# Kernel tuning notes

Hardware: AMD Instinct MI355X
Metric: run time of the kernel (lower is better)

The kernel has to match this reference:

```python
import jax, jax.numpy as jnp
import numpy as np

N_NODES = 50000
N_EDGES = 800000
N_GRAPHS = 128
IN, HID, OUT, CLS = 128, 128, 128, 10


def setup_inputs() -> dict:
    key = jax.random.key(0)
    ks = jax.random.split(key, 16)
    d = {}
    d["features"] = jax.random.normal(ks[0], (N_NODES, IN), jnp.float32)
    d["edge_src"] = jax.random.randint(ks[1], (N_EDGES,), 0, N_NODES)
    d["edge_dst"] = jax.random.randint(ks[2], (N_EDGES,), 0, N_NODES)
    d["graph_ids"] = jnp.sort(jax.random.randint(ks[3], (N_NODES,), 0, N_GRAPHS))

    def lin(k, i, o):
        return (jax.random.normal(k, (i, o), jnp.float32) / np.float32(np.sqrt(i)))

    dims = [(IN, HID), (HID, HID), (HID, OUT)]
    for l, (i, o) in enumerate(dims):
        d[f"Ws{l}"] = lin(ks[4 + 3 * l], i, o)
        d[f"Wn{l}"] = lin(ks[5 + 3 * l], i, o)
        d[f"b{l}"] = jnp.zeros((o,), jnp.float32)
    d["Wf"] = lin(ks[13], OUT, CLS)
    d["bf"] = jnp.zeros((CLS,), jnp.float32)
    return d


def _sage_mean_layer(h, edge_src, edge_dst, Ws, Wn, b, in_deg):
    # mean-aggregate in-neighbor features: gather at src, segment-sum at dst
    msg_sum = jax.ops.segment_sum(h[edge_src], edge_dst, num_segments=N_NODES)
    h_neigh = msg_sum / in_deg  # [N, d], zero-degree nodes divide by 1 -> 0
    return jax.nn.relu(h @ Ws + h_neigh @ Wn + b)


def reference(features, edge_src, edge_dst, graph_ids,
              Ws0, Wn0, b0, Ws1, Wn1, b1, Ws2, Wn2, b2, Wf, bf):
    ones = jnp.ones((N_EDGES,), jnp.float32)
    in_deg = jax.ops.segment_sum(ones, edge_dst, num_segments=N_NODES)
    in_deg = jnp.maximum(in_deg, 1.0)[:, None]  # [N, 1]

    h = features
    h = _sage_mean_layer(h, edge_src, edge_dst, Ws0, Wn0, b0, in_deg)
    h = _sage_mean_layer(h, edge_src, edge_dst, Ws1, Wn1, b1, in_deg)
    h = _sage_mean_layer(h, edge_src, edge_dst, Ws2, Wn2, b2, in_deg)

    # mean graph pooling over node segments
    node_ones = jnp.ones((N_NODES,), jnp.float32)
    counts = jax.ops.segment_sum(node_ones, graph_ids, num_segments=N_GRAPHS)
    counts = jnp.maximum(counts, 1.0)[:, None]
    pooled = jax.ops.segment_sum(h, graph_ids, num_segments=N_GRAPHS) / counts

    return pooled @ Wf + bf  # [N_GRAPHS, CLS]
```

## Files before the change

### kernel.cpp

```cpp
#include <hip/hip_runtime.h>

#define N_NODES  50000
#define N_EDGES  800000
#define N_GRAPHS 128
#define HD       128
#define K2       256
#define CLS      10
#define NB_SCAN  ((N_NODES + 255) / 256)
#define NPART    8
#define PSIZE    (N_NODES / NPART)
#define NBIN     1600
#define CHUNK    (N_EDGES / NBIN)
#define PCAP     131072

typedef __attribute__((ext_vector_type(8))) _Float16 f16x8;
typedef __attribute__((ext_vector_type(4))) float f32x4;
typedef __attribute__((ext_vector_type(2))) float f32x2;

union U4H8 { uint4 u; _Float16 h[8]; };
union U2H4 { uint2 u; _Float16 h[4]; };

typedef const __attribute__((address_space(1))) void* gptr_t;
typedef __attribute__((address_space(3))) void* lptr_t;
#define GLOAD_LDS16(g, l) \
    __builtin_amdgcn_global_load_lds((gptr_t)(g), (lptr_t)(l), 16, 0, 0)

__global__ __launch_bounds__(256) void k_zero(int* __restrict__ z) {
    int i = blockIdx.x * 256 + threadIdx.x;
    if (i < 50008) z[i] = 0;
}

__global__ __launch_bounds__(256) void k_initbin(
    const float* __restrict__ f, unsigned short* __restrict__ c0, unsigned char* __restrict__ f8,
    const float* __restrict__ Ws0, const float* __restrict__ Wn0,
    const float* __restrict__ Ws1, const float* __restrict__ Wn1,
    const float* __restrict__ Ws2, const float* __restrict__ Wn2,
    unsigned short* __restrict__ wt, float* __restrict__ pooled,
    const int* __restrict__ gid, float* __restrict__ counts, int* __restrict__ bflag,
    const int* __restrict__ src, const int* __restrict__ dst,
    unsigned* __restrict__ stag, int* __restrict__ gcount, int* __restrict__ deg) {
    if (blockIdx.x < NBIN) {
        __shared__ int lcount[NPART];
        __shared__ int lbase[NPART];
        const int tid = threadIdx.x;
        const int lo = blockIdx.x * CHUNK;
        if (tid < NPART) lcount[tid] = 0;
        __syncthreads();
        int dc[2], sc[2];
#pragma unroll
        for (int it = 0; it < 2; ++it) {
            int i = lo + tid + it * 256;
            dc[it] = -1;
            if (i < lo + CHUNK) {
                int d = dst[i];
                dc[it] = d; sc[it] = src[i];
                atomicAdd(&deg[d], 1);
                atomicAdd(&lcount[d / PSIZE], 1);
            }
        }
        __syncthreads();
        if (tid < NPART) {
            lbase[tid] = atomicAdd(&gcount[tid], lcount[tid]);
            lcount[tid] = 0;
        }
        __syncthreads();
#pragma unroll
        for (int it = 0; it < 2; ++it) {
            if (dc[it] >= 0) {
                int p = dc[it] / PSIZE;
                int slot = atomicAdd(&lcount[p], 1);
                stag[(size_t)p * PCAP + lbase[p] + slot] =
                    (unsigned)sc[it] | ((unsigned)(dc[it] - p * PSIZE) << 16);
            }
        }
        return;
    }
    long long gi = (long long)(blockIdx.x - NBIN) * 256 + threadIdx.x;
    if (gi < 800000) {
        int t = (int)gi;
        int row = t >> 4, c8 = (t & 15) * 8;
        const float* p = f + (size_t)row * HD + c8;
        float4 a = *(const float4*)p;
        float4 b = *(const float4*)(p + 4);
        U4H8 v;
        v.h[0] = (_Float16)a.x; v.h[1] = (_Float16)a.y;
        v.h[2] = (_Float16)a.z; v.h[3] = (_Float16)a.w;
        v.h[4] = (_Float16)b.x; v.h[5] = (_Float16)b.y;
        v.h[6] = (_Float16)b.z; v.h[7] = (_Float16)b.w;
        *(uint4*)(c0 + (size_t)row * K2 + c8) = v.u;
        int p0 = __builtin_amdgcn_cvt_pk_fp8_f32(a.x, a.y, 0, false);
        p0 = __builtin_amdgcn_cvt_pk_fp8_f32(a.z, a.w, p0, true);
        int p1 = __builtin_amdgcn_cvt_pk_fp8_f32(b.x, b.y, 0, false);
        p1 = __builtin_amdgcn_cvt_pk_fp8_f32(b.z, b.w, p1, true);
        *(uint2*)(f8 + (size_t)row * HD + c8) = make_uint2((unsigned)p0, (unsigned)p1);
        return;
    }
    gi -= 800000;
    if (gi < 3 * HD * K2) {
        int t = (int)gi;
        int l = t / (HD * K2), r = t % (HD * K2);
        int n = r / K2, k = r % K2;
        const float* Ws = (l == 0) ? Ws0 : (l == 1) ? Ws1 : Ws2;
        const float* Wn = (l == 0) ? Wn0 : (l == 1) ? Wn1 : Wn2;
        float w = (k < HD) ? Ws[k * HD + n] : Wn[(k - HD) * HD + n];
        union { unsigned short u; _Float16 h; } c;
        c.h = (_Float16)w;
        wt[t] = c.u;
        return;
    }
    gi -= 3 * HD * K2;
    if (gi < N_GRAPHS * HD) { pooled[gi] = 0.f; return; }
    gi -= (long long)N_GRAPHS * HD;
    if (gi < N_GRAPHS) {
        int g = (int)gi;
        int lo = 0, hi = N_NODES;
        while (lo < hi) { int mid = (lo + hi) >> 1; if (gid[mid] < g) lo = mid + 1; else hi = mid; }
        int start = lo;
        lo = 0; hi = N_NODES;
        while (lo < hi) { int mid = (lo + hi) >> 1; if (gid[mid] <= g) lo = mid + 1; else hi = mid; }
        counts[g] = (float)(lo - start);
        return;
    }
    gi -= N_GRAPHS;
    if (gi < 256) bflag[gi] = 0;
}
#define INIT_ITEMS (800000 + 3 * HD * K2 + N_GRAPHS * HD + N_GRAPHS + 256)
#define INIT_BLOCKS ((INIT_ITEMS + 255) / 256)

__global__ __launch_bounds__(256) void k_scan(const int* __restrict__ deg,
                                              int* __restrict__ rowptr, int* __restrict__ cursor,
                                              int* __restrict__ bsum, int* __restrict__ bflag) {
    __shared__ int s[256];
    __shared__ int r[256];
    const int tid = threadIdx.x;
    const int b = blockIdx.x;
    const int i = b * 256 + tid;
    int v = (i < N_NODES) ? deg[i] : 0;
    s[tid] = v;
    __syncthreads();
    for (int off = 1; off < 256; off <<= 1) {
        int add = (tid >= off) ? s[tid - off] : 0;
        __syncthreads();
        s[tid] += add;
        __syncthreads();
    }
    if (tid == 255) {
        __hip_atomic_store(&bsum[b], s[255], __ATOMIC_RELAXED, __HIP_MEMORY_SCOPE_AGENT);
        __hip_atomic_store(&bflag[b], 1, __ATOMIC_RELEASE, __HIP_MEMORY_SCOPE_AGENT);
    }
    int agg = 0;
    if (tid < b) {
        while (__hip_atomic_load(&bflag[tid], __ATOMIC_ACQUIRE, __HIP_MEMORY_SCOPE_AGENT) == 0) {}
        agg = __hip_atomic_load(&bsum[tid], __ATOMIC_RELAXED, __HIP_MEMORY_SCOPE_AGENT);
    }
    r[tid] = agg;
    __syncthreads();
    for (int off = 128; off > 0; off >>= 1) {
        if (tid < off) r[tid] += r[tid + off];
        __syncthreads();
    }
    if (i < N_NODES) {
        int val = r[0] + s[tid] - v;
        rowptr[i] = val;
        cursor[i] = val;
    }
    if (b == NB_SCAN - 1 && tid == 0) rowptr[N_NODES] = N_EDGES;
}

__global__ __launch_bounds__(256) void k_fill2(const unsigned* __restrict__ stag, const int* __restrict__ gcount,
                                               int* __restrict__ cursor, int* __restrict__ eidx) {
    const int part = blockIdx.x & (NPART - 1);
    const int blk = blockIdx.x >> 3;
    const int n = gcount[part];
    const unsigned* s = stag + (size_t)part * PCAP;
    for (int i = blk * 256 + threadIdx.x; i < n; i += 64 * 256) {
        unsigned v = s[i];
        int srcv = (int)(v & 0xFFFFu);
        int dstv = part * PSIZE + (int)(v >> 16);
        int pos = atomicAdd(&cursor[dstv], 1);
        eidx[pos] = srcv;
    }
}

__global__ __launch_bounds__(256) void k_gather(const unsigned char* __restrict__ h8,
                                                const int* __restrict__ rowptr,
                                                const int* __restrict__ eidx,
                                                unsigned short* __restrict__ msg) {
    const int node = (blockIdx.x * 256 + threadIdx.x) >> 6;
    const int lane = threadIdx.x & 63;
    if (node >= N_NODES) return;
    const int epar = lane >> 4;
    const int d0 = (lane & 15) * 8;
    const int beg = rowptr[node], end = rowptr[node + 1];
    float acc[8] = {0.f, 0.f, 0.f, 0.f, 0.f, 0.f, 0.f, 0.f};
    int j = beg + epar;
    for (; j + 12 < end; j += 16) {
        int s0 = eidx[j], s1 = eidx[j + 4], s2 = eidx[j + 8], s3 = eidx[j + 12];
        uint2 v0 = *(const uint2*)(h8 + (size_t)s0 * HD + d0);
        uint2 v1 = *(const uint2*)(h8 + (size_t)s1 * HD + d0);
        uint2 v2 = *(const uint2*)(h8 + (size_t)s2 * HD + d0);
        uint2 v3 = *(const uint2*)(h8 + (size_t)s3 * HD + d0);
        f32x2 e;
        e = __builtin_amdgcn_cvt_pk_f32_fp8(v0.x, false); acc[0] += e[0]; acc[1] += e[1];
        e = __builtin_amdgcn_cvt_pk_f32_fp8(v0.x, true);  acc[2] += e[0]; acc[3] += e[1];
        e = __builtin_amdgcn_cvt_pk_f32_fp8(v0.y, false); acc[4] += e[0]; acc[5] += e[1];
        e = __builtin_amdgcn_cvt_pk_f32_fp8(v0.y, true);  acc[6] += e[0]; acc[7] += e[1];
        e = __builtin_amdgcn_cvt_pk_f32_fp8(v1.x, false); acc[0] += e[0]; acc[1] += e[1];
        e = __builtin_amdgcn_cvt_pk_f32_fp8(v1.x, true);  acc[2] += e[0]; acc[3] += e[1];
        e = __builtin_amdgcn_cvt_pk_f32_fp8(v1.y, false); acc[4] += e[0]; acc[5] += e[1];
        e = __builtin_amdgcn_cvt_pk_f32_fp8(v1.y, true);  acc[6] += e[0]; acc[7] += e[1];
        e = __builtin_amdgcn_cvt_pk_f32_fp8(v2.x, false); acc[0] += e[0]; acc[1] += e[1];
        e = __builtin_amdgcn_cvt_pk_f32_fp8(v2.x, true);  acc[2] += e[0]; acc[3] += e[1];
        e = __builtin_amdgcn_cvt_pk_f32_fp8(v2.y, false); acc[4] += e[0]; acc[5] += e[1];
        e = __builtin_amdgcn_cvt_pk_f32_fp8(v2.y, true);  acc[6] += e[0]; acc[7] += e[1];
        e = __builtin_amdgcn_cvt_pk_f32_fp8(v3.x, false); acc[0] += e[0]; acc[1] += e[1];
        e = __builtin_amdgcn_cvt_pk_f32_fp8(v3.x, true);  acc[2] += e[0]; acc[3] += e[1];
        e = __builtin_amdgcn_cvt_pk_f32_fp8(v3.y, false); acc[4] += e[0]; acc[5] += e[1];
        e = __builtin_amdgcn_cvt_pk_f32_fp8(v3.y, true);  acc[6] += e[0]; acc[7] += e[1];
    }
    for (; j < end; j += 4) {
        uint2 v0 = *(const uint2*)(h8 + (size_t)eidx[j] * HD + d0);
        f32x2 e;
        e = __builtin_amdgcn_cvt_pk_f32_fp8(v0.x, false); acc[0] += e[0]; acc[1] += e[1];
        e = __builtin_amdgcn_cvt_pk_f32_fp8(v0.x, true);  acc[2] += e[0]; acc[3] += e[1];
        e = __builtin_amdgcn_cvt_pk_f32_fp8(v0.y, false); acc[4] += e[0]; acc[5] += e[1];
        e = __builtin_amdgcn_cvt_pk_f32_fp8(v0.y, true);  acc[6] += e[0]; acc[7] += e[1];
    }
#pragma unroll
    for (int i = 0; i < 8; ++i) {
        acc[i] += __shfl_xor(acc[i], 16);
        acc[i] += __shfl_xor(acc[i], 32);
    }
    if (epar == 0) {
        float inv = (end > beg) ? 1.0f / (float)(end - beg) : 0.f;
        U4H8 o;
#pragma unroll
        for (int i = 0; i < 8; ++i) o.h[i] = (_Float16)(acc[i] * inv);
        *(uint4*)(msg + (size_t)node * K2 + HD + d0) = o.u;
    }
}

__global__ __launch_bounds__(256) void k_sage(const unsigned short* __restrict__ hin,
                                              const unsigned short* __restrict__ wt,
                                              const float* __restrict__ bias,
                                              unsigned short* __restrict__ hout,
                                              unsigned char* __restrict__ hout8,
                                              int write16) {
    __shared__ __align__(16) _Float16 Ah[2][128 * 64];
    __shared__ __align__(16) _Float16 Bw[2][128 * 64];
    const int tid = threadIdx.x;
    const int wv = tid >> 6, lane = tid & 63;
    const int m0 = blockIdx.x * 128;
    const int m_off = (wv >> 1) * 64, n_off = (wv & 1) * 64;
    const int l15 = lane & 15, q = lane >> 4;

    f32x4 acc[4][4];
#pragma unroll
    for (int a = 0; a < 4; ++a)
#pragma unroll
        for (int b = 0; b < 4; ++b) acc[a][b] = (f32x4){0.f, 0.f, 0.f, 0.f};

    auto stage = [&](int bsel, int kt) {
        const int k0 = kt * 64;
#pragma unroll
        for (int i = 0; i < 4; ++i) {
            int idx = tid + i * 256;
            int row = idx >> 3, c = idx & 7;
            int qs = (c ^ (row & 7)) * 8;
            int gm = m0 + row;
            if (gm < N_NODES)
                GLOAD_LDS16(hin + (size_t)gm * K2 + k0 + qs, &Ah[bsel][idx * 8]);
            GLOAD_LDS16(wt + (size_t)row * K2 + k0 + qs, &Bw[bsel][idx * 8]);
        }
    };

    stage(0, 0);
    __syncthreads();
#pragma unroll
    for (int kt = 0; kt < 4; ++kt) {
        const int b = kt & 1;
        if (kt < 3) stage(b ^ 1, kt + 1);
        f16x8 hf[4][2], wf[4][2];
#pragma unroll
        for (int mt = 0; mt < 4; ++mt) {
            const int row = m_off + mt * 16 + l15;
            const int sw = row & 7;
#pragma unroll
            for (int ks = 0; ks < 2; ++ks)
                hf[mt][ks] = *(const f16x8*)&Ah[b][row * 64 + (((ks * 4 + q) ^ sw) * 8)];
        }
#pragma unroll
        for (int nt = 0; nt < 4; ++nt) {
            const int row = n_off + nt * 16 + l15;
            const int sw = row & 7;
#pragma unroll
            for (int ks = 0; ks < 2; ++ks)
                wf[nt][ks] = *(const f16x8*)&Bw[b][row * 64 + (((ks * 4 + q) ^ sw) * 8)];
        }
#pragma unroll
        for (int mt = 0; mt < 4; ++mt)
#pragma unroll
            for (int nt = 0; nt < 4; ++nt) {
                acc[mt][nt] = __builtin_amdgcn_mfma_f32_16x16x32_f16(wf[nt][0], hf[mt][0], acc[mt][nt], 0, 0, 0);
                acc[mt][nt] = __builtin_amdgcn_mfma_f32_16x16x32_f16(wf[nt][1], hf[mt][1], acc[mt][nt], 0, 0, 0);
            }
        __syncthreads();
    }
#pragma unroll
    for (int nt = 0; nt < 4; ++nt) {
        int n = n_off + nt * 16 + q * 4;
        float4 bv = *(const float4*)(bias + n);
#pragma unroll
        for (int mt = 0; mt < 4; ++mt) {
            int m = m0 + m_off + mt * 16 + l15;
            if (m < N_NODES) {
                f32x4 a = acc[mt][nt];
                float r0 = fmaxf(a[0] + bv.x, 0.f);
                float r1 = fmaxf(a[1] + bv.y, 0.f);
                float r2 = fmaxf(a[2] + bv.z, 0.f);
                float r3 = fmaxf(a[3] + bv.w, 0.f);
                if (write16) {
                    U2H4 v;
                    v.h[0] = (_Float16)r0; v.h[1] = (_Float16)r1;
                    v.h[2] = (_Float16)r2; v.h[3] = (_Float16)r3;
                    *(uint2*)(hout + (size_t)m * K2 + n) = v.u;
                }
                int p = __builtin_amdgcn_cvt_pk_fp8_f32(r0, r1, 0, false);
                p = __builtin_amdgcn_cvt_pk_fp8_f32(r2, r3, p, true);
                *(unsigned int*)(hout8 + (size_t)m * HD + n) = (unsigned)p;
            }
        }
    }
}

__global__ __launch_bounds__(256) void k_pool(const unsigned char* __restrict__ h8,
                                              const int* __restrict__ gid,
                                              float* __restrict__ pooled) {
    const int p2 = (threadIdx.x & 63) * 2;
    const int sl = threadIdx.x >> 6;
    const int n0 = blockIdx.x * 128;
    float a0 = 0.f, a1 = 0.f;
    int cur = -1;
    for (int i = sl; i < 128; i += 4) {
        int n = n0 + i;
        if (n >= N_NODES) break;
        int g = gid[n];
        if (g != cur) {
            if (cur >= 0) {
                atomicAdd(&pooled[(size_t)cur * HD + p2], a0);
                atomicAdd(&pooled[(size_t)cur * HD + p2 + 1], a1);
            }
            a0 = 0.f; a1 = 0.f;
            cur = g;
        }
        unsigned short v = *(const unsigned short*)(h8 + (size_t)n * HD + p2);
        f32x2 e = __builtin_amdgcn_cvt_pk_f32_fp8((unsigned)v, false);
        a0 += e[0]; a1 += e[1];
    }
    if (cur >= 0) {
        atomicAdd(&pooled[(size_t)cur * HD + p2], a0);
        atomicAdd(&pooled[(size_t)cur * HD + p2 + 1], a1);
    }
}

__global__ __launch_bounds__(256) void k_final(const float* __restrict__ pooled,
                                               const float* __restrict__ counts,
                                               const float* __restrict__ Wf,
                                               const float* __restrict__ bf,
                                               float* __restrict__ out) {
    int t = blockIdx.x * 256 + threadIdx.x;
    if (t >= N_GRAPHS * CLS) return;
    int g = t / CLS, c = t % CLS;
    float inv = 1.0f / fmaxf(counts[g], 1.0f);
    float s = 0.f;
    for (int k = 0; k < HD; ++k) s += pooled[(size_t)g * HD + k] * Wf[k * CLS + c];
    out[t] = s * inv + bf[c];
}

extern "C" void kernel_launch(void* const* d_in, const int* in_sizes, int n_in,
                              void* d_out, int out_size, void* d_ws, size_t ws_size,
                              hipStream_t stream) {
    const float* features = (const float*)d_in[0];
    const int*   esrc     = (const int*)d_in[1];
    const int*   edst     = (const int*)d_in[2];
    const int*   gids     = (const int*)d_in[3];
    const float* bs[3]  = {(const float*)d_in[6], (const float*)d_in[9], (const float*)d_in[12]};
    const float* Wf = (const float*)d_in[13];
    const float* bfv = (const float*)d_in[14];
    float* out = (float*)d_out;

    int* deg_i  = (int*)d_ws;
    int* gcount = deg_i + 50000;
    int* rowptr = deg_i + 50064;
    int* cursor = rowptr + 50064;
    int* bsum   = cursor + 50048;
    int* bflag  = bsum + 256;
    int* eidx   = bflag + 256;
    unsigned* stag = (unsigned*)(eidx + 800000);
    float* pooled = (float*)(stag + (size_t)NPART * PCAP);
    float* counts = pooled + N_GRAPHS * HD;
    unsigned short* C0 = (unsigned short*)(counts + 128);
    unsigned short* C1 = C0 + (size_t)N_NODES * K2;
    unsigned short* C2 = C1 + (size_t)N_NODES * K2;
    unsigned short* Wt = C2 + (size_t)N_NODES * K2;
    unsigned char* F0 = (unsigned char*)(Wt + 3 * HD * K2);
    unsigned char* F1 = F0 + (size_t)N_NODES * HD;
    unsigned char* F2 = F1 + (size_t)N_NODES * HD;

    k_zero<<<196, 256, 0, stream>>>(deg_i);

    k_initbin<<<NBIN + INIT_BLOCKS, 256, 0, stream>>>(
        features, C0, F0,
        (const float*)d_in[4], (const float*)d_in[5],
        (const float*)d_in[7], (const float*)d_in[8],
        (const float*)d_in[10], (const float*)d_in[11],
        Wt, pooled, gids, counts, bflag,
        esrc, edst, stag, gcount, deg_i);

    k_scan<<<NB_SCAN, 256, 0, stream>>>(deg_i, rowptr, cursor, bsum, bflag);
    k_fill2<<<NPART * 64, 256, 0, stream>>>(stag, gcount, cursor, eidx);

    unsigned short* C[4] = {C0, C1, C2, C0};
    unsigned char* F[4] = {F0, F1, F2, F0};
    for (int l = 0; l < 3; ++l) {
        k_gather<<<(N_NODES * 64 + 255) / 256, 256, 0, stream>>>(F[l], rowptr, eidx, C[l]);
        k_sage<<<(N_NODES + 127) / 128, 256, 0, stream>>>(
            C[l], Wt + (size_t)l * HD * K2, bs[l], C[l + 1], F[l + 1], (l < 2) ? 1 : 0);
    }

    k_pool<<<(N_NODES + 127) / 128, 256, 0, stream>>>(F0, gids, pooled);
    k_final<<<(N_GRAPHS * CLS + 255) / 256, 256, 0, stream>>>(pooled, counts, Wf, bfv, out);
}
```

Measured before the change: 339.4 us.

## Build CSR per partition sub-range with LDS histograms instead of global degree atomics

Removes the global degree atomics, the decoupled-lookback scan kernel and the global-cursor fill kernel. In their place, one k_build kernel runs 64 blocks, one per (partition, sub-range) pair. Each block scans its whole partition's staged edges twice: once to build an LDS histogram and count the edges that fall before its range, then to scatter source indices using LDS atomics. This cuts launches and global atomic traffic, but each block rereads its partition's edge list (about 100k entries) twice, and only 64 blocks are active.

```diff
diff --git a/kernel.cpp b/kernel.cpp
--- a/kernel.cpp
+++ b/kernel.cpp
@@ -6,9 +6,10 @@
 #define HD       128
 #define K2       256
 #define CLS      10
-#define NB_SCAN  ((N_NODES + 255) / 256)
 #define NPART    8
 #define PSIZE    (N_NODES / NPART)
+#define SUB      8
+#define SUBSZ    784
 #define NBIN     1600
 #define CHUNK    (N_EDGES / NBIN)
 #define PCAP     131072
@@ -25,9 +26,8 @@
 #define GLOAD_LDS16(g, l) \
     __builtin_amdgcn_global_load_lds((gptr_t)(g), (lptr_t)(l), 16, 0, 0)
 
-__global__ __launch_bounds__(256) void k_zero(int* __restrict__ z) {
-    int i = blockIdx.x * 256 + threadIdx.x;
-    if (i < 50008) z[i] = 0;
+__global__ __launch_bounds__(64) void k_zero(int* __restrict__ z) {
+    if (threadIdx.x < 8) z[threadIdx.x] = 0;
 }
 
 __global__ __launch_bounds__(256) void k_initbin(
@@ -36,9 +36,9 @@
     const float* __restrict__ Ws1, const float* __restrict__ Wn1,
     const float* __restrict__ Ws2, const float* __restrict__ Wn2,
     unsigned short* __restrict__ wt, float* __restrict__ pooled,
-    const int* __restrict__ gid, float* __restrict__ counts, int* __restrict__ bflag,
+    const int* __restrict__ gid, float* __restrict__ counts,
     const int* __restrict__ src, const int* __restrict__ dst,
-    unsigned* __restrict__ stag, int* __restrict__ gcount, int* __restrict__ deg) {
+    unsigned* __restrict__ stag, int* __restrict__ gcount) {
     if (blockIdx.x < NBIN) {
         __shared__ int lcount[NPART];
         __shared__ int lbase[NPART];
@@ -54,7 +54,6 @@
             if (i < lo + CHUNK) {
                 int d = dst[i];
                 dc[it] = d; sc[it] = src[i];
-                atomicAdd(&deg[d], 1);
                 atomicAdd(&lcount[d / PSIZE], 1);
             }
         }
@@ -119,67 +118,98 @@
         lo = 0; hi = N_NODES;
         while (lo < hi) { int mid = (lo + hi) >> 1; if (gid[mid] <= g) lo = mid + 1; else hi = mid; }
         counts[g] = (float)(lo - start);
-        return;
-    }
-    gi -= N_GRAPHS;
-    if (gi < 256) bflag[gi] = 0;
-}
-#define INIT_ITEMS (800000 + 3 * HD * K2 + N_GRAPHS * HD + N_GRAPHS + 256)
+    }
+}
+#define INIT_ITEMS (800000 + 3 * HD * K2 + N_GRAPHS * HD + N_GRAPHS)
 #define INIT_BLOCKS ((INIT_ITEMS + 255) / 256)
 
-__global__ __launch_bounds__(256) void k_scan(const int* __restrict__ deg,
-                                              int* __restrict__ rowptr, int* __restrict__ cursor,
-                                              int* __restrict__ bsum, int* __restrict__ bflag) {
-    __shared__ int s[256];
-    __shared__ int r[256];
+__global__ __launch_bounds__(512) void k_build(const unsigned* __restrict__ stag,
+                                               const int* __restrict__ gcount,
+                                               int* __restrict__ rowptr, int* __restrict__ eidx) {
+    __shared__ int hist[SUBSZ];
+    __shared__ int sc[512];
+    __shared__ int before_sh;
+    __shared__ int base_sh;
     const int tid = threadIdx.x;
-    const int b = blockIdx.x;
-    const int i = b * 256 + tid;
-    int v = (i < N_NODES) ? deg[i] : 0;
-    s[tid] = v;
+    const int p = blockIdx.x & (NPART - 1);
+    const int s = blockIdx.x >> 3;
+    const int lo = s * SUBSZ;
+    const int hi = min(lo + SUBSZ, PSIZE);
+    for (int j = tid; j < SUBSZ; j += 512) hist[j] = 0;
+    if (tid == 0) {
+        int b = 0;
+        for (int q = 0; q < p; ++q) b += gcount[q];
+        base_sh = b;
+        before_sh = 0;
+    }
     __syncthreads();
-    for (int off = 1; off < 256; off <<= 1) {
-        int add = (tid >= off) ? s[tid - off] : 0;
-        __syncthreads();
-        s[tid] += add;
-        __syncthreads();
-    }
-    if (tid == 255) {
-        __hip_atomic_store(&bsum[b], s[255], __ATOMIC_RELAXED, __HIP_MEMORY_SCOPE_AGENT);
-        __hip_atomic_store(&bflag[b], 1, __ATOMIC_RELEASE, __HIP_MEMORY_SCOPE_AGENT);
-    }
-    int agg = 0;
-    if (tid < b) {
-        while (__hip_atomic_load(&bflag[tid], __ATOMIC_ACQUIRE, __HIP_MEMORY_SCOPE_AGENT) == 0) {}
-        agg = __hip_atomic_load(&bsum[tid], __ATOMIC_RELAXED, __HIP_MEMORY_SCOPE_AGENT);
-    }
-    r[tid] = agg;
+    const int n = gcount[p];
+    const unsigned* sp = stag + (size_t)p * PCAP;
+    int bef = 0;
+    const int nmain = (n / 2048) * 2048;
+    for (int i = tid; i < nmain; i += 2048) {
+        unsigned v0 = sp[i], v1 = sp[i + 512], v2 = sp[i + 1024], v3 = sp[i + 1536];
+#pragma unroll
+        for (int u = 0; u < 4; ++u) {
+            int off = (int)((u == 0 ? v0 : u == 1 ? v1 : u == 2 ? v2 : v3) >> 16);
+            if (off >= lo && off < hi) atomicAdd(&hist[off - lo], 1);
+            bef += (off < lo) ? 1 : 0;
+        }
+    }
+    for (int i = nmain + tid; i < n; i += 512) {
+        int off = (int)(sp[i] >> 16);
+        if (off >= lo && off < hi) atomicAdd(&hist[off - lo], 1);
+        bef += (off < lo) ? 1 : 0;
+    }
+#pragma unroll
+    for (int d = 1; d < 64; d <<= 1) bef += __shfl_xor(bef, d);
+    if ((tid & 63) == 0 && bef) atomicAdd(&before_sh, bef);
     __syncthreads();
-    for (int off = 128; off > 0; off >>= 1) {
-        if (tid < off) r[tid] += r[tid + off];
-        __syncthreads();
-    }
-    if (i < N_NODES) {
-        int val = r[0] + s[tid] - v;
-        rowptr[i] = val;
-        cursor[i] = val;
-    }
-    if (b == NB_SCAN - 1 && tid == 0) rowptr[N_NODES] = N_EDGES;
-}
-
-__global__ __launch_bounds__(256) void k_fill2(const unsigned* __restrict__ stag, const int* __restrict__ gcount,
-                                               int* __restrict__ cursor, int* __restrict__ eidx) {
-    const int part = blockIdx.x & (NPART - 1);
-    const int blk = blockIdx.x >> 3;
-    const int n = gcount[part];
-    const unsigned* s = stag + (size_t)part * PCAP;
-    for (int i = blk * 256 + threadIdx.x; i < n; i += 64 * 256) {
-        unsigned v = s[i];
-        int srcv = (int)(v & 0xFFFFu);
-        int dstv = part * PSIZE + (int)(v >> 16);
-        int pos = atomicAdd(&cursor[dstv], 1);
-        eidx[pos] = srcv;
-    }
+    const int T2 = tid * 2;
+    int lsum = 0;
+    if (T2 < SUBSZ) lsum = hist[T2] + hist[T2 + 1];
+    sc[tid] = lsum;
+    __syncthreads();
+    for (int off = 1; off < 512; off <<= 1) {
+        int add = (tid >= off) ? sc[tid - off] : 0;
+        __syncthreads();
+        sc[tid] += add;
+        __syncthreads();
+    }
+    const int run0 = sc[tid] - lsum;
+    const int B = base_sh + before_sh;
+    if (T2 < SUBSZ) {
+        int h0 = hist[T2];
+        int h1 = hist[T2 + 1];
+        hist[T2] = run0;
+        hist[T2 + 1] = run0 + h0;
+        int n0 = lo + T2, n1 = lo + T2 + 1;
+        if (n0 < PSIZE) rowptr[p * PSIZE + n0] = B + run0;
+        if (n1 < PSIZE) rowptr[p * PSIZE + n1] = B + run0 + h0;
+        (void)h1;
+    }
+    __syncthreads();
+    for (int i = tid; i < nmain; i += 2048) {
+        unsigned v0 = sp[i], v1 = sp[i + 512], v2 = sp[i + 1024], v3 = sp[i + 1536];
+#pragma unroll
+        for (int u = 0; u < 4; ++u) {
+            unsigned v = (u == 0 ? v0 : u == 1 ? v1 : u == 2 ? v2 : v3);
+            int off = (int)(v >> 16);
+            if (off >= lo && off < hi) {
+                int slot = atomicAdd(&hist[off - lo], 1);
+                eidx[B + slot] = (int)(v & 0xFFFFu);
+            }
+        }
+    }
+    for (int i = nmain + tid; i < n; i += 512) {
+        unsigned v = sp[i];
+        int off = (int)(v >> 16);
+        if (off >= lo && off < hi) {
+            int slot = atomicAdd(&hist[off - lo], 1);
+            eidx[B + slot] = (int)(v & 0xFFFFu);
+        }
+    }
+    if (blockIdx.x == 8 * SUB - 1 && tid == 0) rowptr[N_NODES] = N_EDGES;
 }
 
 __global__ __launch_bounds__(256) void k_gather(const unsigned char* __restrict__ h8,
@@ -389,13 +419,9 @@
     const float* bfv = (const float*)d_in[14];
     float* out = (float*)d_out;
 
-    int* deg_i  = (int*)d_ws;
-    int* gcount = deg_i + 50000;
-    int* rowptr = deg_i + 50064;
-    int* cursor = rowptr + 50064;
-    int* bsum   = cursor + 50048;
-    int* bflag  = bsum + 256;
-    int* eidx   = bflag + 256;
+    int* gcount = (int*)d_ws;
+    int* rowptr = gcount + 8;
+    int* eidx   = rowptr + 50008;
     unsigned* stag = (unsigned*)(eidx + 800000);
     float* pooled = (float*)(stag + (size_t)NPART * PCAP);
     float* counts = pooled + N_GRAPHS * HD;
@@ -407,18 +433,17 @@
     unsigned char* F1 = F0 + (size_t)N_NODES * HD;
     unsigned char* F2 = F1 + (size_t)N_NODES * HD;
 
-    k_zero<<<196, 256, 0, stream>>>(deg_i);
+    k_zero<<<1, 64, 0, stream>>>(gcount);
 
     k_initbin<<<NBIN + INIT_BLOCKS, 256, 0, stream>>>(
         features, C0, F0,
         (const float*)d_in[4], (const float*)d_in[5],
         (const float*)d_in[7], (const float*)d_in[8],
         (const float*)d_in[10], (const float*)d_in[11],
-        Wt, pooled, gids, counts, bflag,
-        esrc, edst, stag, gcount, deg_i);
-
-    k_scan<<<NB_SCAN, 256, 0, stream>>>(deg_i, rowptr, cursor, bsum, bflag);
-    k_fill2<<<NPART * 64, 256, 0, stream>>>(stag, gcount, cursor, eidx);
+        Wt, pooled, gids, counts,
+        esrc, edst, stag, gcount);
+
+    k_build<<<NPART * SUB, 512, 0, stream>>>(stag, gcount, rowptr, eidx);
 
     unsigned short* C[4] = {C0, C1, C2, C0};
     unsigned char* F[4] = {F0, F1, F2, F0};
```

Measured after the change: 319.5 us. -5.9%, faster.

## Build CSR via per-partition LDS histograms and LDS-cursor scatter

Applied to the files above, without the earlier changes.

Replaces the global degree atomics and global-cursor atomic fill with a two-pass counting sort. Each of 128 blocks (8 partitions × 16 sub-chunks) first builds a shared-memory histogram of destination offsets. The scan then sums those histograms and writes per-block starting cursors. The scatter pass uses shared-memory atomics for slot assignment, removing contended global atomics. In exchange it adds a kernel, a large ghist buffer, and extra reads of the staged edges, with only 128 blocks doing the work.

```diff
diff --git a/kernel.cpp b/kernel.cpp
--- a/kernel.cpp
+++ b/kernel.cpp
@@ -6,9 +6,10 @@
 #define HD       128
 #define K2       256
 #define CLS      10
-#define NB_SCAN  ((N_NODES + 255) / 256)
 #define NPART    8
 #define PSIZE    (N_NODES / NPART)
+#define NSUB     16
+#define NB_SCAN  ((N_NODES + 255) / 256)
 #define NBIN     1600
 #define CHUNK    (N_EDGES / NBIN)
 #define PCAP     131072
@@ -25,9 +26,8 @@
 #define GLOAD_LDS16(g, l) \
     __builtin_amdgcn_global_load_lds((gptr_t)(g), (lptr_t)(l), 16, 0, 0)
 
-__global__ __launch_bounds__(256) void k_zero(int* __restrict__ z) {
-    int i = blockIdx.x * 256 + threadIdx.x;
-    if (i < 50008) z[i] = 0;
+__global__ __launch_bounds__(64) void k_zero(int* __restrict__ z) {
+    if (threadIdx.x < 8) z[threadIdx.x] = 0;
 }
 
 __global__ __launch_bounds__(256) void k_initbin(
@@ -38,7 +38,7 @@
     unsigned short* __restrict__ wt, float* __restrict__ pooled,
     const int* __restrict__ gid, float* __restrict__ counts, int* __restrict__ bflag,
     const int* __restrict__ src, const int* __restrict__ dst,
-    unsigned* __restrict__ stag, int* __restrict__ gcount, int* __restrict__ deg) {
+    unsigned* __restrict__ stag, int* __restrict__ gcount) {
     if (blockIdx.x < NBIN) {
         __shared__ int lcount[NPART];
         __shared__ int lbase[NPART];
@@ -54,7 +54,6 @@
             if (i < lo + CHUNK) {
                 int d = dst[i];
                 dc[it] = d; sc[it] = src[i];
-                atomicAdd(&deg[d], 1);
                 atomicAdd(&lcount[d / PSIZE], 1);
             }
         }
@@ -127,25 +126,54 @@
 #define INIT_ITEMS (800000 + 3 * HD * K2 + N_GRAPHS * HD + N_GRAPHS + 256)
 #define INIT_BLOCKS ((INIT_ITEMS + 255) / 256)
 
-__global__ __launch_bounds__(256) void k_scan(const int* __restrict__ deg,
-                                              int* __restrict__ rowptr, int* __restrict__ cursor,
+__global__ __launch_bounds__(512) void k_hist(const unsigned* __restrict__ stag,
+                                              const int* __restrict__ gcount,
+                                              int* __restrict__ ghist) {
+    __shared__ int hist[PSIZE];
+    const int tid = threadIdx.x;
+    const int p = blockIdx.x & (NPART - 1);
+    const int s = blockIdx.x >> 3;
+    for (int j = tid; j < PSIZE; j += 512) hist[j] = 0;
+    __syncthreads();
+    const int n = gcount[p];
+    const int cs = (int)(((long long)s * n) / NSUB);
+    const int ce = (int)(((long long)(s + 1) * n) / NSUB);
+    const unsigned* sp = stag + (size_t)p * PCAP;
+    for (int i = cs + tid; i < ce; i += 512)
+        atomicAdd(&hist[sp[i] >> 16], 1);
+    __syncthreads();
+    int* gh = ghist + (size_t)blockIdx.x * PSIZE;
+    for (int j = tid; j < PSIZE; j += 512) gh[j] = hist[j];
+}
+
+__global__ __launch_bounds__(256) void k_scan(int* __restrict__ ghist,
+                                              int* __restrict__ rowptr,
                                               int* __restrict__ bsum, int* __restrict__ bflag) {
-    __shared__ int s[256];
+    __shared__ int sc[256];
     __shared__ int r[256];
     const int tid = threadIdx.x;
     const int b = blockIdx.x;
-    const int i = b * 256 + tid;
-    int v = (i < N_NODES) ? deg[i] : 0;
-    s[tid] = v;
-    __syncthreads();
-    for (int off = 1; off < 256; off <<= 1) {
-        int add = (tid >= off) ? s[tid - off] : 0;
-        __syncthreads();
-        s[tid] += add;
+    const int node = b * 256 + tid;
+    int d[NSUB];
+    int deg = 0, p = 0, off = 0;
+    if (node < N_NODES) {
+        p = node / PSIZE; off = node - p * PSIZE;
+#pragma unroll
+        for (int s = 0; s < NSUB; ++s) {
+            d[s] = ghist[(size_t)(s * NPART + p) * PSIZE + off];
+            deg += d[s];
+        }
+    }
+    sc[tid] = deg;
+    __syncthreads();
+    for (int o = 1; o < 256; o <<= 1) {
+        int add = (tid >= o) ? sc[tid - o] : 0;
+        __syncthreads();
+        sc[tid] += add;
         __syncthreads();
     }
     if (tid == 255) {
-        __hip_atomic_store(&bsum[b], s[255], __ATOMIC_RELAXED, __HIP_MEMORY_SCOPE_AGENT);
+        __hip_atomic_store(&bsum[b], sc[255], __ATOMIC_RELAXED, __HIP_MEMORY_SCOPE_AGENT);
         __hip_atomic_store(&bflag[b], 1, __ATOMIC_RELEASE, __HIP_MEMORY_SCOPE_AGENT);
     }
     int agg = 0;
@@ -155,30 +183,42 @@
     }
     r[tid] = agg;
     __syncthreads();
-    for (int off = 128; off > 0; off >>= 1) {
-        if (tid < off) r[tid] += r[tid + off];
-        __syncthreads();
-    }
-    if (i < N_NODES) {
-        int val = r[0] + s[tid] - v;
-        rowptr[i] = val;
-        cursor[i] = val;
+    for (int o = 128; o > 0; o >>= 1) {
+        if (tid < o) r[tid] += r[tid + o];
+        __syncthreads();
+    }
+    if (node < N_NODES) {
+        int base = r[0] + sc[tid] - deg;
+        rowptr[node] = base;
+        int c = base;
+#pragma unroll
+        for (int s = 0; s < NSUB; ++s) {
+            ghist[(size_t)(s * NPART + p) * PSIZE + off] = c;
+            c += d[s];
+        }
     }
     if (b == NB_SCAN - 1 && tid == 0) rowptr[N_NODES] = N_EDGES;
 }
 
-__global__ __launch_bounds__(256) void k_fill2(const unsigned* __restrict__ stag, const int* __restrict__ gcount,
-                                               int* __restrict__ cursor, int* __restrict__ eidx) {
-    const int part = blockIdx.x & (NPART - 1);
-    const int blk = blockIdx.x >> 3;
-    const int n = gcount[part];
-    const unsigned* s = stag + (size_t)part * PCAP;
-    for (int i = blk * 256 + threadIdx.x; i < n; i += 64 * 256) {
-        unsigned v = s[i];
-        int srcv = (int)(v & 0xFFFFu);
-        int dstv = part * PSIZE + (int)(v >> 16);
-        int pos = atomicAdd(&cursor[dstv], 1);
-        eidx[pos] = srcv;
+__global__ __launch_bounds__(512) void k_scatter(const unsigned* __restrict__ stag,
+                                                 const int* __restrict__ gcount,
+                                                 const int* __restrict__ ghist,
+                                                 int* __restrict__ eidx) {
+    __shared__ int cur[PSIZE];
+    const int tid = threadIdx.x;
+    const int p = blockIdx.x & (NPART - 1);
+    const int s = blockIdx.x >> 3;
+    const int* gh = ghist + (size_t)blockIdx.x * PSIZE;
+    for (int j = tid; j < PSIZE; j += 512) cur[j] = gh[j];
+    __syncthreads();
+    const int n = gcount[p];
+    const int cs = (int)(((long long)s * n) / NSUB);
+    const int ce = (int)(((long long)(s + 1) * n) / NSUB);
+    const unsigned* sp = stag + (size_t)p * PCAP;
+    for (int i = cs + tid; i < ce; i += 512) {
+        unsigned v = sp[i];
+        int slot = atomicAdd(&cur[v >> 16], 1);
+        eidx[slot] = (int)(v & 0xFFFFu);
     }
 }
 
@@ -389,15 +429,14 @@
     const float* bfv = (const float*)d_in[14];
     float* out = (float*)d_out;
 
-    int* deg_i  = (int*)d_ws;
-    int* gcount = deg_i + 50000;
-    int* rowptr = deg_i + 50064;
-    int* cursor = rowptr + 50064;
-    int* bsum   = cursor + 50048;
+    int* gcount = (int*)d_ws;
+    int* rowptr = gcount + 8;
+    int* bsum   = rowptr + 50008;
     int* bflag  = bsum + 256;
     int* eidx   = bflag + 256;
     unsigned* stag = (unsigned*)(eidx + 800000);
-    float* pooled = (float*)(stag + (size_t)NPART * PCAP);
+    int* ghist  = (int*)(stag + (size_t)NPART * PCAP);
+    float* pooled = (float*)(ghist + (size_t)NPART * NSUB * PSIZE);
     float* counts = pooled + N_GRAPHS * HD;
     unsigned short* C0 = (unsigned short*)(counts + 128);
     unsigned short* C1 = C0 + (size_t)N_NODES * K2;
@@ -407,7 +446,7 @@
     unsigned char* F1 = F0 + (size_t)N_NODES * HD;
     unsigned char* F2 = F1 + (size_t)N_NODES * HD;
 
-    k_zero<<<196, 256, 0, stream>>>(deg_i);
+    k_zero<<<1, 64, 0, stream>>>(gcount);
 
     k_initbin<<<NBIN + INIT_BLOCKS, 256, 0, stream>>>(
         features, C0, F0,
@@ -415,10 +454,11 @@
         (const float*)d_in[7], (const float*)d_in[8],
         (const float*)d_in[10], (const float*)d_in[11],
         Wt, pooled, gids, counts, bflag,
-        esrc, edst, stag, gcount, deg_i);
-
-    k_scan<<<NB_SCAN, 256, 0, stream>>>(deg_i, rowptr, cursor, bsum, bflag);
-    k_fill2<<<NPART * 64, 256, 0, stream>>>(stag, gcount, cursor, eidx);
+        esrc, edst, stag, gcount);
+
+    k_hist<<<NPART * NSUB, 512, 0, stream>>>(stag, gcount, ghist);
+    k_scan<<<NB_SCAN, 256, 0, stream>>>(ghist, rowptr, bsum, bflag);
+    k_scatter<<<NPART * NSUB, 512, 0, stream>>>(stag, gcount, ghist, eidx);
 
     unsigned short* C[4] = {C0, C1, C2, C0};
     unsigned char* F[4] = {F0, F1, F2, F0};
```

New measurement: 296.8 us. -12.6%, faster.
